# Kernel tuning notes

Measured on AMD Instinct MI355X. Metric: run time of the kernel, lower is better.

Reference implementation:

```python
import jax, jax.numpy as jnp
import numpy as np

B, N, IN_CH = 4, 8192, 4
K = 16
W0, W1, W2 = 64, 128, 256
NUM_CLASSES = 3


def setup_inputs() -> dict:
    key = jax.random.key(0)
    ks = jax.random.split(key, 16)

    def lin(kw, kb, fan_in, fan_out):
        bound = 1.0 / np.sqrt(fan_in)
        w = jax.random.uniform(kw, (fan_in, fan_out), jnp.float32, -bound, bound)
        b = jax.random.uniform(kb, (fan_out,), jnp.float32, -bound, bound)
        return w, b

    x = jax.random.normal(ks[0], (B, N, IN_CH), jnp.float32)
    stem_w, stem_b = lin(ks[1], ks[2], IN_CH, W0)
    b1_w, b1_b = lin(ks[3], ks[4], 2 * W0 + 3, W1)
    b2_w, b2_b = lin(ks[5], ks[6], 2 * W1 + 3, W2)
    glob_w, glob_b = lin(ks[7], ks[8], W2, W2)
    head1_w, head1_b = lin(ks[9], ks[10], 2 * W2, W2)
    head2_w, head2_b = lin(ks[11], ks[12], W2, NUM_CLASSES)
    return {
        'x': x,
        'hmix_a': jnp.float32(1.0), 'hmix_b': jnp.float32(1.0), 'hmix_c': jnp.float32(0.0),
        'stem_w': stem_w, 'stem_b': stem_b,
        'b1_w': b1_w, 'b1_b': b1_b,
        'b2_w': b2_w, 'b2_b': b2_b,
        'glob_w': glob_w, 'glob_b': glob_b,
        'head1_w': head1_w, 'head1_b': head1_b,
        'head2_w': head2_w, 'head2_b': head2_b,
        'thresh': jnp.float32(0.15), 'sharp': jnp.float32(10.0), 'scale': jnp.float32(0.5),
    }


def _knn_idx(coords, k):
    # coords: [B,N,3] -> idx of k nearest neighbors (incl. self), no grad.
    c = jax.lax.stop_gradient(coords)
    xx = jnp.sum(c * c, axis=-1, keepdims=True)            # [B,N,1]
    dist = xx + jnp.swapaxes(xx, 1, 2) - 2.0 * jnp.einsum('bnc,bmc->bnm', c, c)
    dist = jnp.maximum(dist, 0.0)
    _, idx = jax.lax.top_k(-dist, k)                       # smallest distances
    return idx                                             # [B,N,k]


def _local_agg(coords, feat, idx, w, b):
    # gather-concat-MLP-maxpool, faithful to LocalAggBlock (pool='max')
    bidx = jnp.arange(coords.shape[0])[:, None, None]
    nb_f = feat[bidx, idx]                                 # [B,N,k,C]
    nb_p = coords[bidx, idx]                               # [B,N,k,3]
    fi = feat[:, :, None, :]
    pi = coords[:, :, None, :]
    h = jnp.concatenate(
        [jnp.broadcast_to(fi, nb_f.shape), nb_f - fi, nb_p - pi], axis=-1)
    h = jax.nn.relu(jnp.einsum('bnkd,do->bnko', h, w) + b)
    return jnp.max(h, axis=2)                              # [B,N,out]


def reference(x, hmix_a, hmix_b, hmix_c, stem_w, stem_b, b1_w, b1_b,
              b2_w, b2_b, glob_w, glob_b, head1_w, head1_b,
              head2_w, head2_b, thresh, sharp, scale):
    # HeightMixer: z_eff = a*z + b*hag + c
    z_eff = hmix_a * x[..., 2] + hmix_b * x[..., 3] + hmix_c
    coords = jnp.stack([x[..., 0], x[..., 1], z_eff], axis=-1)  # [B,N,3]

    f = jax.nn.relu(x @ stem_w + stem_b)                   # stem: [B,N,64]

    # both blocks use the same coords -> same KNN graph; compute once
    idx = _knn_idx(coords, K)
    f = _local_agg(coords, f, idx, b1_w, b1_b)             # [B,N,128]
    f = _local_agg(coords, f, idx, b2_w, b2_b)             # [B,N,256]

    g = jnp.max(f, axis=1)                                 # [B,256]
    g = jax.nn.relu(g @ glob_w + glob_b)
    g = jnp.broadcast_to(g[:, None, :], f.shape)           # [B,N,256]

    h = jnp.concatenate([f, g], axis=-1)                   # [B,N,512]
    h = jax.nn.relu(h @ head1_w + head1_b)
    logits = h @ head2_w + head2_b                         # [B,N,3]

    # HeightPriorBias on class 0
    hag = x[..., 3]
    bias = scale * jax.nn.sigmoid(sharp * (thresh - hag))
    logits = logits.at[..., 0].add(bias)
    return logits
```

## Files before the change

### kernel.cpp

```cpp
#include <hip/hip_runtime.h>
#include <math.h>

typedef unsigned long long u64;
typedef unsigned int u32;
typedef _Float16 h8v __attribute__((ext_vector_type(8)));
typedef float    f4v __attribute__((ext_vector_type(4)));
typedef float    f2v __attribute__((ext_vector_type(2)));

#define MFMA16(a,b,c) __builtin_amdgcn_mfma_f32_16x16x32_f16(a, b, c, 0, 0, 0)

#define B_ 4
#define N_ 8192
#define K_ 16
#define W0_ 64
#define W1_ 128
#define W2_ 256
#define X0_ 96
#define X1_ 160

__global__ __launch_bounds__(256) void prep_kernel(
    const float* __restrict__ x,
    const float* __restrict__ stem_w, const float* __restrict__ stem_b,
    const float* __restrict__ hmix_a, const float* __restrict__ hmix_b,
    const float* __restrict__ hmix_c,
    float* __restrict__ coords4, _Float16* __restrict__ fx0,
    _Float16* __restrict__ fx1,
    const float* __restrict__ b1_w, const float* __restrict__ b2_w,
    const float* __restrict__ h1w,
    _Float16* __restrict__ w1m, _Float16* __restrict__ w1d,
    _Float16* __restrict__ w2m, _Float16* __restrict__ w2d,
    _Float16* __restrict__ h1wT, float* __restrict__ part) {
  const int bi = blockIdx.x;
  const int tid = threadIdx.x;
  const int PB = (B_*N_)/4;
  if (bi < PB) {
    const int p = bi * 4 + (tid >> 6);
    const int o = tid & 63;
    const float x0 = x[p*4+0], x1 = x[p*4+1], x2 = x[p*4+2], x3 = x[p*4+3];
    const float z = hmix_a[0]*x2 + hmix_b[0]*x3 + hmix_c[0];
    float acc = stem_b[o] + x0*stem_w[0*W0_+o] + x1*stem_w[1*W0_+o]
              + x2*stem_w[2*W0_+o] + x3*stem_w[3*W0_+o];
    fx0[p*X0_+o] = (_Float16)fmaxf(acc, 0.f);
    if (o < 32) {
      const float tv = (o==0) ? x0 : (o==1) ? x1 : (o==2) ? z : 0.f;
      fx0[p*X0_+W0_+o] = (_Float16)tv;
      fx1[(size_t)p*X1_+W1_+o] = (_Float16)tv;
    }
    if (o == 0) {
      const float xx = x0*x0 + x1*x1 + z*z;
      ((float4*)coords4)[p] = make_float4(x0, x1, z, xx);
    }
  } else if (bi < PB + W1_) {
    const int o = bi - PB, c = tid;
    if (c < X0_) {
      float mv = 0.f, dv = 0.f;
      if (c < W0_)        { const float wm = b1_w[(W0_+c)*W1_+o]; mv = wm; dv = b1_w[c*W1_+o] - wm; }
      else if (c < W0_+3) { const float wp = b1_w[(2*W0_+(c-W0_))*W1_+o]; mv = wp; dv = -wp; }
      w1m[o*X0_+c] = (_Float16)mv;
      w1d[o*X0_+c] = (_Float16)dv;
    }
  } else if (bi < PB + W1_ + W2_) {
    const int o = bi - PB - W1_, c = tid;
    if (c < X1_) {
      float mv = 0.f, dv = 0.f;
      if (c < W1_)        { const float wm = b2_w[(W1_+c)*W2_+o]; mv = wm; dv = b2_w[c*W2_+o] - wm; }
      else if (c < W1_+3) { const float wp = b2_w[(2*W1_+(c-W1_))*W2_+o]; mv = wp; dv = -wp; }
      w2m[o*X1_+c] = (_Float16)mv;
      w2d[o*X1_+c] = (_Float16)dv;
    }
  } else if (bi < PB + W1_ + 2*W2_) {
    const int o = bi - PB - W1_ - W2_;
    for (int c = tid; c < 512; c += 256)
      h1wT[(size_t)o*512 + c] = (_Float16)h1w[(size_t)c*256 + o];
  } else {
    ((float4*)part)[tid] = make_float4(0.f, 0.f, 0.f, 0.f);
  }
}

#define DPP_SHR1(v) __builtin_amdgcn_update_dpp(0, (v), 0x138, 0xF, 0xF, false)

#define DPP_MIN(v, ctrl)                                                        \
  { const int _t = __builtin_amdgcn_update_dpp(__float_as_int(v),               \
      __float_as_int(v), ctrl, 0xF, 0xF, false);                                \
    v = fminf(v, __int_as_float(_t)); }

__device__ __forceinline__ float sixteenth_of_minima(float v) {
  float th = 0.f;
#pragma unroll
  for (int r = 0; r < 16; ++r) {
    float w = v;
    DPP_MIN(w, 0x111); DPP_MIN(w, 0x112); DPP_MIN(w, 0x114); DPP_MIN(w, 0x118);
    DPP_MIN(w, 0x142); DPP_MIN(w, 0x143);
    const float mv = __int_as_float(
        __builtin_amdgcn_readlane(__float_as_int(w), 63));
    th = mv;
    v = (v == mv) ? INFINITY : v;
  }
  return th;
}

#define KNN_EVT(d, dk, ik)                                                      \
  {                                                                             \
    const int s = (int)__ffsll((unsigned long long)m) - 1;  m &= m - 1;         \
    const float dc = __int_as_float(__builtin_amdgcn_readlane(                  \
                       __float_as_int(d), s));                                  \
    const bool cnd = dc < dk;                                                   \
    const u64 cm = __ballot(cnd) << 1;                                          \
    const float pd = __int_as_float(DPP_SHR1(__float_as_int(dk)));              \
    const int   pi = DPP_SHR1(ik);                                              \
    const bool pc = (cm >> lane) & 1;                                           \
    dk = cnd ? (pc ? pd : dc) : dk;                                             \
    ik = cnd ? (pc ? pi : (jbase + s)) : ik;                                    \
  }

#define KNN_CHUNK(d, dk, ik, T, Th)                                             \
  { u64 m = __ballot(d <= T);                                                   \
    if (m) {                                                                    \
      do { KNN_EVT(d, dk, ik) } while (m);                                      \
      T = fminf(Th, __int_as_float(__builtin_amdgcn_readlane(                   \
            __float_as_int(dk), 15)));                                          \
    }                                                                           \
  }

#define KNN_DIST2(dA, dB)                                                       \
  const f2v cjx = {cj.x, cj.x}, cjy = {cj.y, cj.y},                             \
            cjz = {cj.z, cj.z}, cjw = {cj.w, cj.w};                             \
  f2v tA = cAx * cjx;                                                           \
  tA = __builtin_elementwise_fma(cAy, cjy, tA);                                 \
  tA = __builtin_elementwise_fma(cAz, cjz, tA);                                 \
  const f2v dA = __builtin_elementwise_fma(tA, m2, cAw + cjw);                  \
  f2v tB = cBx * cjx;                                                           \
  tB = __builtin_elementwise_fma(cBy, cjy, tB);                                 \
  tB = __builtin_elementwise_fma(cBz, cjz, tB);                                 \
  const f2v dB = __builtin_elementwise_fma(tB, m2, cBw + cjw);

__global__ __launch_bounds__(256, 8) void knn_kernel(
    const float* __restrict__ coords4, int* __restrict__ knn_idx) {
  const int tid = threadIdx.x;
  const int wid = tid >> 6;
  const int lane = tid & 63;
  const int p0 = blockIdx.x * 16 + wid * 4;
  const int b = p0 >> 13;
  const float4* cb = ((const float4*)coords4) + (b << 13);
  const float4 c0 = ((const float4*)coords4)[p0+0];
  const float4 c1 = ((const float4*)coords4)[p0+1];
  const float4 c2 = ((const float4*)coords4)[p0+2];
  const float4 c3 = ((const float4*)coords4)[p0+3];
  const f2v m2 = {-2.f, -2.f};
  const f2v cAx = {c0.x, c1.x}, cAy = {c0.y, c1.y}, cAz = {c0.z, c1.z}, cAw = {c0.w, c1.w};
  const f2v cBx = {c2.x, c3.x}, cBy = {c2.y, c3.y}, cBz = {c2.z, c3.z}, cBw = {c2.w, c3.w};

  float lm0 = INFINITY, lm1 = INFINITY, lm2 = INFINITY, lm3 = INFINITY;
  for (int it = 0; it < 32; ++it) {
    const float4 cj = cb[it*64 + lane];
    KNN_DIST2(dA, dB)
    lm0 = fminf(lm0, fmaxf(dA[0], 0.f));
    lm1 = fminf(lm1, fmaxf(dA[1], 0.f));
    lm2 = fminf(lm2, fmaxf(dB[0], 0.f));
    lm3 = fminf(lm3, fmaxf(dB[1], 0.f));
  }
  const float Th0 = sixteenth_of_minima(lm0);
  const float Th1 = sixteenth_of_minima(lm1);
  const float Th2 = sixteenth_of_minima(lm2);
  const float Th3 = sixteenth_of_minima(lm3);

  float dk0 = INFINITY, dk1 = INFINITY, dk2 = INFINITY, dk3 = INFINITY;
  int   ik0 = 0, ik1 = 0, ik2 = 0, ik3 = 0;
  float T0 = Th0, T1 = Th1, T2 = Th2, T3 = Th3;

  for (int it = 0; it < N_/64; ++it) {
    const int jbase = it*64;
    const float4 cj = cb[jbase + lane];
    KNN_DIST2(dA, dB)
    const float d0 = fmaxf(dA[0], 0.f);
    const float d1 = fmaxf(dA[1], 0.f);
    const float d2 = fmaxf(dB[0], 0.f);
    const float d3 = fmaxf(dB[1], 0.f);
    KNN_CHUNK(d0, dk0, ik0, T0, Th0);
    KNN_CHUNK(d1, dk1, ik1, T1, Th1);
    KNN_CHUNK(d2, dk2, ik2, T2, Th2);
    KNN_CHUNK(d3, dk3, ik3, T3, Th3);
  }

  if (lane < K_) {
    knn_idx[(size_t)(p0+0)*K_ + lane] = ik0;
    knn_idx[(size_t)(p0+1)*K_ + lane] = ik1;
    knn_idx[(size_t)(p0+2)*K_ + lane] = ik2;
    knn_idx[(size_t)(p0+3)*K_ + lane] = ik3;
  }
}

template<int KS, int NPASS, bool GMAX>
__global__ __launch_bounds__(256) void aggm_kernel(
    const _Float16* __restrict__ fx, const int* __restrict__ knn_idx,
    const _Float16* __restrict__ midT, const _Float16* __restrict__ difT,
    const float* __restrict__ bw,
    _Float16* __restrict__ fo, const int ostr, u32* __restrict__ part) {
  const int XD  = KS*32;
  const int XDP = XD + 8;
  const int CH  = KS*4;
  const int p0 = blockIdx.x * 16;
  const int bb = (p0 >> 13) << 13;
  const int tid = threadIdx.x;
  const int w = tid >> 6, lane = tid & 63, col = lane & 15, quad = lane >> 4;
  const int koff = quad * 8;

  __shared__ int s_idx[256];
  __shared__ _Float16 sA[2][64*(KS*32+8)];

  s_idx[tid] = knn_idx[p0*K_ + tid];

  f4v cacc[NPASS][2];
  {
    h8v Ao[KS];
    const _Float16* ap = fx + (size_t)(p0+col)*XD + koff;
#pragma unroll
    for (int kk = 0; kk < KS; ++kk) Ao[kk] = *(const h8v*)(ap + kk*32);
#pragma unroll
    for (int ps = 0; ps < NPASS; ++ps) {
      const int o0 = ps*128 + w*32;
      const _Float16* b0 = difT + (size_t)(o0 + col)*XD + koff;
      const _Float16* b1 = difT + (size_t)(o0 + 16 + col)*XD + koff;
      f4v c0 = {0.f,0.f,0.f,0.f}, c1 = {0.f,0.f,0.f,0.f};
#pragma unroll
      for (int kk = 0; kk < KS; ++kk) {
        c0 = MFMA16(Ao[kk], *(const h8v*)(b0 + kk*32), c0);
        c1 = MFMA16(Ao[kk], *(const h8v*)(b1 + kk*32), c1);
      }
      cacc[ps][0] = c0; cacc[ps][1] = c1;
    }
  }

  h8v Bf[NPASS][2][KS];
  float bias[NPASS][2];
#pragma unroll
  for (int ps = 0; ps < NPASS; ++ps) {
    const int o0 = ps*128 + w*32;
#pragma unroll
    for (int kk = 0; kk < KS; ++kk) {
      Bf[ps][0][kk] = *(const h8v*)(midT + (size_t)(o0 + col)*XD + kk*32 + koff);
      Bf[ps][1][kk] = *(const h8v*)(midT + (size_t)(o0 + 16 + col)*XD + kk*32 + koff);
    }
    bias[ps][0] = bw[o0 + col];
    bias[ps][1] = bw[o0 + 16 + col];
  }
  __syncthreads();

  for (int c = tid; c < 64*CH; c += 256) {
    const int r = c / CH, o = c - r*CH;
    *(uint4*)&sA[0][r*XDP + o*8] =
        *(const uint4*)(fx + (size_t)(bb + s_idx[((r&15)<<4) + (r>>4)])*XD + o*8);
  }
  __syncthreads();

  f4v M[NPASS][2];
#pragma unroll
  for (int ps = 0; ps < NPASS; ++ps) {
    M[ps][0] = (f4v){-INFINITY,-INFINITY,-INFINITY,-INFINITY};
    M[ps][1] = (f4v){-INFINITY,-INFINITY,-INFINITY,-INFINITY};
  }

  for (int s = 0; s < 4; ++s) {
    const int buf = s & 1;
    if (s < 3) {
      for (int c = tid; c < 64*CH; c += 256) {
        const int r = c / CH, o = c - r*CH;
        *(uint4*)&sA[buf^1][r*XDP + o*8] =
            *(const uint4*)(fx + (size_t)(bb + s_idx[((r&15)<<4) + 4*s+4 + (r>>4)])*XD + o*8);
      }
    }
#pragma unroll
    for (int half = 0; half < 4; ++half) {
      h8v Ac[KS];
      const _Float16* ap = &sA[buf][(half*16 + col)*XDP + koff];
#pragma unroll
      for (int kk = 0; kk < KS; ++kk) Ac[kk] = *(const h8v*)(ap + kk*32);
#pragma unroll
      for (int ps = 0; ps < NPASS; ++ps) {
        f4v d0 = {0.f,0.f,0.f,0.f}, d1 = {0.f,0.f,0.f,0.f};
#pragma unroll
        for (int kk = 0; kk < KS; ++kk) {
          d0 = MFMA16(Ac[kk], Bf[ps][0][kk], d0);
          d1 = MFMA16(Ac[kk], Bf[ps][1][kk], d1);
        }
#pragma unroll
        for (int e = 0; e < 4; ++e) {
          M[ps][0][e] = fmaxf(M[ps][0][e], d0[e]);
          M[ps][1][e] = fmaxf(M[ps][1][e], d1[e]);
        }
      }
    }
    if (s < 3) __syncthreads();
  }

  const int prow = p0 + (quad << 2);
  const int bq = p0 >> 13;
#pragma unroll
  for (int ps = 0; ps < NPASS; ++ps) {
    const int o0 = ps*128 + w*32;
    const int oa = o0 + col, ob = oa + 16;
    float v0[4], v1[4];
#pragma unroll
    for (int reg = 0; reg < 4; ++reg) {
      v0[reg] = fmaxf(M[ps][0][reg] + cacc[ps][0][reg] + bias[ps][0], 0.f);
      v1[reg] = fmaxf(M[ps][1][reg] + cacc[ps][1][reg] + bias[ps][1], 0.f);
      fo[(size_t)(prow+reg)*ostr + oa] = (_Float16)v0[reg];
      fo[(size_t)(prow+reg)*ostr + ob] = (_Float16)v1[reg];
    }
    if (GMAX) {
      float bm0 = fmaxf(fmaxf(v0[0], v0[1]), fmaxf(v0[2], v0[3]));
      float bm1 = fmaxf(fmaxf(v1[0], v1[1]), fmaxf(v1[2], v1[3]));
      bm0 = fmaxf(bm0, __shfl_xor(bm0, 16, 64));
      bm0 = fmaxf(bm0, __shfl_xor(bm0, 32, 64));
      bm1 = fmaxf(bm1, __shfl_xor(bm1, 16, 64));
      bm1 = fmaxf(bm1, __shfl_xor(bm1, 32, 64));
      if (quad == 0) {
        atomicMax(part + bq*W2_ + oa, __float_as_uint(bm0));
        atomicMax(part + bq*W2_ + ob, __float_as_uint(bm1));
      }
    }
  }
}

__global__ __launch_bounds__(256) void gfc_kernel(
    const float* __restrict__ part, const float* __restrict__ gw,
    const float* __restrict__ gb, _Float16* __restrict__ g2h) {
  const int b = blockIdx.x;
  const int o = threadIdx.x;
  __shared__ float s_g[W2_];
  s_g[o] = part[b*W2_ + o];
  __syncthreads();
  float acc = gb[o];
  for (int d = 0; d < W2_; ++d) acc += s_g[d]*gw[d*W2_ + o];
  g2h[b*W2_ + o] = (_Float16)fmaxf(acc, 0.f);
}

__global__ __launch_bounds__(256) void headm_kernel(
    const _Float16* __restrict__ f2h, const _Float16* __restrict__ g2h,
    const _Float16* __restrict__ h1wT, const float* __restrict__ h1b,
    const float* __restrict__ h2w, const float* __restrict__ h2b,
    const float* __restrict__ x,
    const float* __restrict__ thresh, const float* __restrict__ sharp,
    const float* __restrict__ scale,
    float* __restrict__ out) {
  const int p0 = blockIdx.x * 32;
  const int b = p0 >> 13;
  const int tid = threadIdx.x;
  const int w = tid >> 6, lane = tid & 63, col = lane & 15, quad = lane >> 4;

  __shared__ _Float16 sA[32*520];
  __shared__ float    sh[32*260];

  for (int t = tid; t < 32*32; t += 256) {
    const int r = t >> 5, cc = (t & 31) * 8;
    *(uint4*)&sA[r*520 + cc] = *(const uint4*)&f2h[(size_t)(p0+r)*W2_ + cc];
  }
  for (int t = tid; t < 32*32; t += 256) {
    const int r = t >> 5, cc = (t & 31) * 8;
    *(uint4*)&sA[r*520 + 256 + cc] = *(const uint4*)&g2h[b*W2_ + cc];
  }
  __syncthreads();

  f4v acc[2][4];
#pragma unroll
  for (int r = 0; r < 2; ++r)
#pragma unroll
    for (int t = 0; t < 4; ++t) acc[r][t] = (f4v){0.f,0.f,0.f,0.f};

  for (int kk = 0; kk < 16; ++kk) {
    const h8v a0 = *(const h8v*)&sA[col*520 + kk*32 + quad*8];
    const h8v a1 = *(const h8v*)&sA[(16+col)*520 + kk*32 + quad*8];
#pragma unroll
    for (int t = 0; t < 4; ++t) {
      const h8v bt = *(const h8v*)&h1wT[(size_t)(w*64 + t*16 + col)*512 + kk*32 + quad*8];
      acc[0][t] = MFMA16(a0, bt, acc[0][t]);
      acc[1][t] = MFMA16(a1, bt, acc[1][t]);
    }
  }
#pragma unroll
  for (int r = 0; r < 2; ++r)
#pragma unroll
    for (int t = 0; t < 4; ++t) {
      const int o = w*64 + t*16 + col;
      const float bv = h1b[o];
#pragma unroll
      for (int reg = 0; reg < 4; ++reg)
        sh[(r*16 + quad*4 + reg)*260 + o] = fmaxf(acc[r][t][reg] + bv, 0.f);
    }
  __syncthreads();

  if (tid < 96) {
    const int pp = tid / 3, c = tid % 3;
    float s = h2b[c];
    for (int d = 0; d < 256; ++d) s += sh[pp*260 + d] * h2w[d*3 + c];
    if (c == 0) {
      const float hag = x[(size_t)(p0+pp)*4 + 3];
      s += scale[0] / (1.f + expf(-sharp[0]*(thresh[0] - hag)));
    }
    out[(size_t)(p0+pp)*3 + c] = s;
  }
}

extern "C" void kernel_launch(void* const* d_in, const int* in_sizes, int n_in,
                              void* d_out, int out_size, void* d_ws, size_t ws_size,
                              hipStream_t stream) {
  const float* x       = (const float*)d_in[0];
  const float* hmix_a  = (const float*)d_in[1];
  const float* hmix_b  = (const float*)d_in[2];
  const float* hmix_c  = (const float*)d_in[3];
  const float* stem_w  = (const float*)d_in[4];
  const float* stem_b  = (const float*)d_in[5];
  const float* b1_w    = (const float*)d_in[6];
  const float* b1_b    = (const float*)d_in[7];
  const float* b2_w    = (const float*)d_in[8];
  const float* b2_b    = (const float*)d_in[9];
  const float* glob_w  = (const float*)d_in[10];
  const float* glob_b  = (const float*)d_in[11];
  const float* head1_w = (const float*)d_in[12];
  const float* head1_b = (const float*)d_in[13];
  const float* head2_w = (const float*)d_in[14];
  const float* head2_b = (const float*)d_in[15];
  const float* thresh  = (const float*)d_in[16];
  const float* sharp   = (const float*)d_in[17];
  const float* scale   = (const float*)d_in[18];
  float* out = (float*)d_out;

  char* base = (char*)d_ws;
  float*     coords4 = (float*)    (base + 0);
  int*       idxb    = (int*)      (base + 524288);
  _Float16*  fx0     = (_Float16*) (base + 2621440);
  _Float16*  fx1     = (_Float16*) (base + 8912896);
  _Float16*  f2h     = (_Float16*) (base + 19398656);
  _Float16*  w1m     = (_Float16*) (base + 36175872);
  _Float16*  w1d     = (_Float16*) (base + 36200448);
  _Float16*  w2m     = (_Float16*) (base + 36225024);
  _Float16*  w2d     = (_Float16*) (base + 36306944);
  _Float16*  h1wT    = (_Float16*) (base + 36388864);
  float*     part    = (float*)    (base + 36651008);
  _Float16*  g2h     = (_Float16*) (base + 36782080);
  const int NP = B_ * N_;

  prep_kernel<<<NP/4 + W1_ + 2*W2_ + 1, 256, 0, stream>>>(
      x, stem_w, stem_b, hmix_a, hmix_b, hmix_c, coords4, fx0, fx1,
      b1_w, b2_w, head1_w, w1m, w1d, w2m, w2d, h1wT, part);
  knn_kernel<<<NP/16, 256, 0, stream>>>(coords4, idxb);
  aggm_kernel<3, 1, false><<<NP/16, 256, 0, stream>>>(
      fx0, idxb, w1m, w1d, b1_b, fx1, X1_, (u32*)0);
  aggm_kernel<5, 2, true><<<NP/16, 256, 0, stream>>>(
      fx1, idxb, w2m, w2d, b2_b, f2h, W2_, (u32*)part);
  gfc_kernel<<<B_, 256, 0, stream>>>(part, glob_w, glob_b, g2h);
  headm_kernel<<<NP/32, 256, 0, stream>>>(f2h, g2h, h1wT, head1_b, head2_w, head2_b,
                                          x, thresh, sharp, scale, out);
}
```

Before: 411.2 us.

## Compute KNN distances with split-fp16 MFMA and LDS candidate filtering

Rewrites the KNN kernel so that pairwise distance terms come from MFMA 16x16x32 fp16 products. Coordinates are split into hi/lo fp16 parts so the products keep near-fp32 accuracy. Candidates under a per-query threshold, taken from the minima of 64-point strided samples with a small slack, are appended to per-query LDS lists via atomics. The 16 nearest are then picked by repeated wave-wide min reductions with index tie-breaking. This removes the serial per-event ballot/DPP insertion loop and moves the dense distance work onto matrix cores. The risks are overflow past the 128-entry cap, slight precision differences that could change neighbour choice, and lower occupancy from the larger LDS footprint.

```diff
diff --git a/kernel.cpp b/kernel.cpp
--- a/kernel.cpp
+++ b/kernel.cpp
@@ -17,6 +17,8 @@
 #define W2_ 256
 #define X0_ 96
 #define X1_ 160
+#define QAD_ 32
+#define CAP_ 128
 
 __global__ __launch_bounds__(256) void prep_kernel(
     const float* __restrict__ x,
@@ -29,7 +31,9 @@
     const float* __restrict__ h1w,
     _Float16* __restrict__ w1m, _Float16* __restrict__ w1d,
     _Float16* __restrict__ w2m, _Float16* __restrict__ w2d,
-    _Float16* __restrict__ h1wT, float* __restrict__ part) {
+    _Float16* __restrict__ h1wT,
+    _Float16* __restrict__ qa, _Float16* __restrict__ cbq,
+    float* __restrict__ part) {
   const int bi = blockIdx.x;
   const int tid = threadIdx.x;
   const int PB = (B_*N_)/4;
@@ -49,6 +53,41 @@
     if (o == 0) {
       const float xx = x0*x0 + x1*x1 + z*z;
       ((float4*)coords4)[p] = make_float4(x0, x1, z, xx);
+    } else if (o == 1) {
+      const _Float16 hx = (_Float16)x0, hy = (_Float16)x1, hz = (_Float16)z;
+      const _Float16 lx = (_Float16)(x0 - (float)hx);
+      const _Float16 ly = (_Float16)(x1 - (float)hy);
+      const _Float16 lz = (_Float16)(z  - (float)hz);
+      const _Float16 one = (_Float16)1.f, Z = (_Float16)0.f;
+      h8v a0 = {hx, hy, hz, lx, ly, lz, hx, hy};
+      h8v a1 = {hz, lx, ly, lz, one, one, Z, Z};
+      h8v zr = {Z,Z,Z,Z,Z,Z,Z,Z};
+      *(h8v*)(qa + (size_t)p*QAD_)      = a0;
+      *(h8v*)(qa + (size_t)p*QAD_ + 8)  = a1;
+      *(h8v*)(qa + (size_t)p*QAD_ + 16) = zr;
+      *(h8v*)(qa + (size_t)p*QAD_ + 24) = zr;
+    } else if (o == 2) {
+      const _Float16 hx = (_Float16)x0, hy = (_Float16)x1, hz = (_Float16)z;
+      const _Float16 lx = (_Float16)(x0 - (float)hx);
+      const _Float16 ly = (_Float16)(x1 - (float)hy);
+      const _Float16 lz = (_Float16)(z  - (float)hz);
+      const float xx = x0*x0 + x1*x1 + z*z;
+      const _Float16 xh = (_Float16)xx;
+      const _Float16 xl = (_Float16)(xx - (float)xh);
+      const _Float16 nhx = (_Float16)(-2.f*(float)hx);
+      const _Float16 nhy = (_Float16)(-2.f*(float)hy);
+      const _Float16 nhz = (_Float16)(-2.f*(float)hz);
+      const _Float16 nlx = (_Float16)(-2.f*(float)lx);
+      const _Float16 nly = (_Float16)(-2.f*(float)ly);
+      const _Float16 nlz = (_Float16)(-2.f*(float)lz);
+      const _Float16 Z = (_Float16)0.f;
+      h8v b0 = {nhx, nhy, nhz, nlx, nly, nlz, nlx, nly};
+      h8v b1 = {nlz, nhx, nhy, nhz, xh, xl, Z, Z};
+      h8v zr = {Z,Z,Z,Z,Z,Z,Z,Z};
+      *(h8v*)(cbq + (size_t)p*QAD_)      = b0;
+      *(h8v*)(cbq + (size_t)p*QAD_ + 8)  = b1;
+      *(h8v*)(cbq + (size_t)p*QAD_ + 16) = zr;
+      *(h8v*)(cbq + (size_t)p*QAD_ + 24) = zr;
     }
   } else if (bi < PB + W1_) {
     const int o = bi - PB, c = tid;
@@ -77,11 +116,9 @@
   }
 }
 
-#define DPP_SHR1(v) __builtin_amdgcn_update_dpp(0, (v), 0x138, 0xF, 0xF, false)
-
 #define DPP_MIN(v, ctrl)                                                        \
-  { const int _t = __builtin_amdgcn_update_dpp(__float_as_int(v),               \
-      __float_as_int(v), ctrl, 0xF, 0xF, false);                                \
+  { const int _t = __builtin_amdgcn_update_dpp(0, __float_as_int(v),            \
+      ctrl, 0xF, 0xF, false);                                                   \
     v = fminf(v, __int_as_float(_t)); }
 
 __device__ __forceinline__ float sixteenth_of_minima(float v) {
@@ -98,29 +135,6 @@
   }
   return th;
 }
-
-#define KNN_EVT(d, dk, ik)                                                      \
-  {                                                                             \
-    const int s = (int)__ffsll((unsigned long long)m) - 1;  m &= m - 1;         \
-    const float dc = __int_as_float(__builtin_amdgcn_readlane(                  \
-                       __float_as_int(d), s));                                  \
-    const bool cnd = dc < dk;                                                   \
-    const u64 cm = __ballot(cnd) << 1;                                          \
-    const float pd = __int_as_float(DPP_SHR1(__float_as_int(dk)));              \
-    const int   pi = DPP_SHR1(ik);                                              \
-    const bool pc = (cm >> lane) & 1;                                           \
-    dk = cnd ? (pc ? pd : dc) : dk;                                             \
-    ik = cnd ? (pc ? pi : (jbase + s)) : ik;                                    \
-  }
-
-#define KNN_CHUNK(d, dk, ik, T, Th)                                             \
-  { u64 m = __ballot(d <= T);                                                   \
-    if (m) {                                                                    \
-      do { KNN_EVT(d, dk, ik) } while (m);                                      \
-      T = fminf(Th, __int_as_float(__builtin_amdgcn_readlane(                   \
-            __float_as_int(dk), 15)));                                          \
-    }                                                                           \
-  }
 
 #define KNN_DIST2(dA, dB)                                                       \
   const f2v cjx = {cj.x, cj.x}, cjy = {cj.y, cj.y},                             \
@@ -134,24 +148,34 @@
   tB = __builtin_elementwise_fma(cBz, cjz, tB);                                 \
   const f2v dB = __builtin_elementwise_fma(tB, m2, cBw + cjw);
 
-__global__ __launch_bounds__(256, 8) void knn_kernel(
-    const float* __restrict__ coords4, int* __restrict__ knn_idx) {
+__global__ __launch_bounds__(256, 4) void knn_kernel(
+    const float* __restrict__ coords4, const _Float16* __restrict__ qa,
+    const _Float16* __restrict__ cbq, int* __restrict__ knn_idx) {
   const int tid = threadIdx.x;
   const int wid = tid >> 6;
   const int lane = tid & 63;
-  const int p0 = blockIdx.x * 16 + wid * 4;
-  const int b = p0 >> 13;
-  const float4* cb = ((const float4*)coords4) + (b << 13);
-  const float4 c0 = ((const float4*)coords4)[p0+0];
-  const float4 c1 = ((const float4*)coords4)[p0+1];
-  const float4 c2 = ((const float4*)coords4)[p0+2];
-  const float4 c3 = ((const float4*)coords4)[p0+3];
+  const int col = lane & 15, quad = lane >> 4;
+  const int p0 = blockIdx.x * 16;
+  const int bb = (p0 >> 13) << 13;
+
+  __shared__ float s_Tp[16];
+  __shared__ int   s_cnt[16];
+  __shared__ float s_ld[16][CAP_];
+  __shared__ int   s_li[16][CAP_];
+  if (tid < 16) s_cnt[tid] = 0;
+
+  const float4* cb = ((const float4*)coords4) + bb;
+  const int q0 = p0 + wid * 4;
+  const float4 c0 = ((const float4*)coords4)[q0+0];
+  const float4 c1 = ((const float4*)coords4)[q0+1];
+  const float4 c2 = ((const float4*)coords4)[q0+2];
+  const float4 c3 = ((const float4*)coords4)[q0+3];
   const f2v m2 = {-2.f, -2.f};
   const f2v cAx = {c0.x, c1.x}, cAy = {c0.y, c1.y}, cAz = {c0.z, c1.z}, cAw = {c0.w, c1.w};
   const f2v cBx = {c2.x, c3.x}, cBy = {c2.y, c3.y}, cBz = {c2.z, c3.z}, cBw = {c2.w, c3.w};
 
   float lm0 = INFINITY, lm1 = INFINITY, lm2 = INFINITY, lm3 = INFINITY;
-  for (int it = 0; it < 32; ++it) {
+  for (int it = 0; it < 64; ++it) {
     const float4 cj = cb[it*64 + lane];
     KNN_DIST2(dA, dB)
     lm0 = fminf(lm0, fmaxf(dA[0], 0.f));
@@ -163,30 +187,68 @@
   const float Th1 = sixteenth_of_minima(lm1);
   const float Th2 = sixteenth_of_minima(lm2);
   const float Th3 = sixteenth_of_minima(lm3);
-
-  float dk0 = INFINITY, dk1 = INFINITY, dk2 = INFINITY, dk3 = INFINITY;
-  int   ik0 = 0, ik1 = 0, ik2 = 0, ik3 = 0;
-  float T0 = Th0, T1 = Th1, T2 = Th2, T3 = Th3;
-
-  for (int it = 0; it < N_/64; ++it) {
-    const int jbase = it*64;
-    const float4 cj = cb[jbase + lane];
-    KNN_DIST2(dA, dB)
-    const float d0 = fmaxf(dA[0], 0.f);
-    const float d1 = fmaxf(dA[1], 0.f);
-    const float d2 = fmaxf(dB[0], 0.f);
-    const float d3 = fmaxf(dB[1], 0.f);
-    KNN_CHUNK(d0, dk0, ik0, T0, Th0);
-    KNN_CHUNK(d1, dk1, ik1, T1, Th1);
-    KNN_CHUNK(d2, dk2, ik2, T2, Th2);
-    KNN_CHUNK(d3, dk3, ik3, T3, Th3);
-  }
-
-  if (lane < K_) {
-    knn_idx[(size_t)(p0+0)*K_ + lane] = ik0;
-    knn_idx[(size_t)(p0+1)*K_ + lane] = ik1;
-    knn_idx[(size_t)(p0+2)*K_ + lane] = ik2;
-    knn_idx[(size_t)(p0+3)*K_ + lane] = ik3;
+  if (lane == 0) {
+    s_Tp[wid*4+0] = Th0 - c0.w + (1e-3f + 1e-5f*c0.w);
+    s_Tp[wid*4+1] = Th1 - c1.w + (1e-3f + 1e-5f*c1.w);
+    s_Tp[wid*4+2] = Th2 - c2.w + (1e-3f + 1e-5f*c2.w);
+    s_Tp[wid*4+3] = Th3 - c3.w + (1e-3f + 1e-5f*c3.w);
+  }
+  __syncthreads();
+
+  const float Tq0 = s_Tp[quad*4+0], Tq1 = s_Tp[quad*4+1],
+              Tq2 = s_Tp[quad*4+2], Tq3 = s_Tp[quad*4+3];
+  const h8v afrag = *(const h8v*)(qa + (size_t)(p0 + col)*QAD_ + quad*8);
+  const int cb0 = wid * 2048;
+  const _Float16* cbp = cbq + (size_t)(bb + cb0 + col)*QAD_ + quad*8;
+
+  h8v bcur = *(const h8v*)cbp;
+#pragma unroll 2
+  for (int t = 0; t < 128; ++t) {
+    const int nx = ((t < 127) ? (t+1) : 0) * 16 * QAD_;
+    const h8v bnxt = *(const h8v*)(cbp + nx);
+    f4v acc = {0.f, 0.f, 0.f, 0.f};
+    acc = MFMA16(afrag, bcur, acc);
+    const int cidx = cb0 + t*16 + col;
+    if (acc[0] < Tq0) { const int pos = atomicAdd(&s_cnt[quad*4+0], 1);
+      if (pos < CAP_) { s_ld[quad*4+0][pos] = acc[0]; s_li[quad*4+0][pos] = cidx; } }
+    if (acc[1] < Tq1) { const int pos = atomicAdd(&s_cnt[quad*4+1], 1);
+      if (pos < CAP_) { s_ld[quad*4+1][pos] = acc[1]; s_li[quad*4+1][pos] = cidx; } }
+    if (acc[2] < Tq2) { const int pos = atomicAdd(&s_cnt[quad*4+2], 1);
+      if (pos < CAP_) { s_ld[quad*4+2][pos] = acc[2]; s_li[quad*4+2][pos] = cidx; } }
+    if (acc[3] < Tq3) { const int pos = atomicAdd(&s_cnt[quad*4+3], 1);
+      if (pos < CAP_) { s_ld[quad*4+3][pos] = acc[3]; s_li[quad*4+3][pos] = cidx; } }
+    bcur = bnxt;
+  }
+  __syncthreads();
+
+  for (int qq = 0; qq < 4; ++qq) {
+    const int q = wid*4 + qq;
+    const int cnt = s_cnt[q];
+    const int L = (cnt < CAP_) ? cnt : CAP_;
+    float d0 = (lane      < L) ? s_ld[q][lane]      : INFINITY;
+    float d1 = (lane + 64 < L) ? s_ld[q][lane + 64] : INFINITY;
+    int   i0 = (lane      < L) ? s_li[q][lane]      : 0x7fffffff;
+    int   i1 = (lane + 64 < L) ? s_li[q][lane + 64] : 0x7fffffff;
+    int keep = 0;
+    for (int r = 0; r < K_; ++r) {
+      float dl = d0; int il = i0; bool s1 = false;
+      if (d1 < dl || (d1 == dl && i1 < il)) { dl = d1; il = i1; s1 = true; }
+      float w = dl;
+      DPP_MIN(w, 0x111); DPP_MIN(w, 0x112); DPP_MIN(w, 0x114); DPP_MIN(w, 0x118);
+      DPP_MIN(w, 0x142); DPP_MIN(w, 0x143);
+      const float dmin = __int_as_float(
+          __builtin_amdgcn_readlane(__float_as_int(w), 63));
+      u64 m = __ballot(dl == dmin);
+      int bi = 0x7fffffff, bl = 0;
+      do {
+        const int s = (int)__ffsll((unsigned long long)m) - 1; m &= m - 1;
+        const int ii = __builtin_amdgcn_readlane(il, s);
+        if (ii < bi) { bi = ii; bl = s; }
+      } while (m);
+      if (lane == bl) { if (s1) d1 = INFINITY; else d0 = INFINITY; }
+      if (lane == r) keep = bi;
+    }
+    if (lane < K_) knn_idx[(size_t)(p0 + q)*K_ + lane] = keep;
   }
 }
 
@@ -431,6 +493,8 @@
   _Float16*  fx0     = (_Float16*) (base + 2621440);
   _Float16*  fx1     = (_Float16*) (base + 8912896);
   _Float16*  f2h     = (_Float16*) (base + 19398656);
+  _Float16*  qa      = (_Float16*) (base + 19398656);
+  _Float16*  cbq     = (_Float16*) (base + 21495808);
   _Float16*  w1m     = (_Float16*) (base + 36175872);
   _Float16*  w1d     = (_Float16*) (base + 36200448);
   _Float16*  w2m     = (_Float16*) (base + 36225024);
@@ -442,8 +506,8 @@
 
   prep_kernel<<<NP/4 + W1_ + 2*W2_ + 1, 256, 0, stream>>>(
       x, stem_w, stem_b, hmix_a, hmix_b, hmix_c, coords4, fx0, fx1,
-      b1_w, b2_w, head1_w, w1m, w1d, w2m, w2d, h1wT, part);
-  knn_kernel<<<NP/16, 256, 0, stream>>>(coords4, idxb);
+      b1_w, b2_w, head1_w, w1m, w1d, w2m, w2d, h1wT, qa, cbq, part);
+  knn_kernel<<<NP/16, 256, 0, stream>>>(coords4, qa, cbq, idxb);
   aggm_kernel<3, 1, false><<<NP/16, 256, 0, stream>>>(
       fx0, idxb, w1m, w1d, b1_b, fx1, X1_, (u32*)0);
   aggm_kernel<5, 2, true><<<NP/16, 256, 0, stream>>>(
```

Result: faster. 394.6 us (-4.0%).
